# Performance work log

Hardware: AMD Instinct MI355X
Metric: run time of the kernel (lower is better)

The kernel has to match this reference:

```python
import jax, jax.numpy as jnp
import numpy as np

VOCAB, E, H, L, N = 32000, 256, 512, 512, 64


def setup_inputs() -> dict:
    key = jax.random.key(0)
    ks = jax.random.split(key, 8)
    s_in = 1.0 / np.sqrt(H + E)
    return {
        "x": jax.random.randint(ks[0], (L, N), 0, VOCAB),
        "emb": jax.random.normal(ks[1], (VOCAB, E), dtype=jnp.float32),
        # weights stored (in, out); math identical to torch Linear with W.T
        "Wz": jax.random.uniform(ks[2], (H + E, H), jnp.float32, -s_in, s_in),
        "bz": jax.random.uniform(ks[3], (H,), jnp.float32, -s_in, s_in),
        "Wr": jax.random.uniform(ks[4], (H + E, H), jnp.float32, -s_in, s_in),
        "br": jax.random.uniform(ks[5], (H,), jnp.float32, -s_in, s_in),
        "Wh": jax.random.uniform(ks[6], (H + E, H), jnp.float32, -s_in, s_in),
        "bh": jax.random.uniform(ks[7], (H,), jnp.float32, -s_in, s_in),
    }


def reference(x, emb, Wz, bz, Wr, br, Wh, bh):
    # x: (L, N) int indices -> embedded once: (L, N, E)
    xe = emb[x]
    h0 = jnp.zeros((x.shape[1], Wz.shape[1]), dtype=emb.dtype)

    def step(h, e_t):
        hx = jnp.concatenate([h, e_t], axis=1)            # (N, H+E)
        z = jax.nn.sigmoid(hx @ Wz + bz)                  # update gate
        r = jax.nn.sigmoid(hx @ Wr + br)                  # reset gate
        rhx = jnp.concatenate([r * h, e_t], axis=1)
        h_tilde = jnp.tanh(rhx @ Wh + bh)
        h_new = (1.0 - z) * h + z * h_tilde
        return h_new, h_new

    _, hs = jax.lax.scan(step, h0, xe)                    # hs: (L, N, H)
    return hs
```

## Files before the change

kernel.cpp:

```cpp
#include <hip/hip_runtime.h>


#define LSTEPS 512
#define NBATCH 64
#define HDIM   512
#define EDIM   256
#define KDIM   768
#define NBLK   32
#define TPB    256

typedef _Float16 f16x8 __attribute__((ext_vector_type(8)));
typedef float    f32x4 __attribute__((ext_vector_type(4)));

__device__ __forceinline__ float sigm(float x){ return 1.0f/(1.0f+__expf(-x)); }
__device__ __forceinline__ float tanh_fast(float x){
  float e = __expf(2.0f*x);
  return 1.0f - 2.0f/(e + 1.0f);
}

__global__ void prep_w(const float* __restrict__ Wz, const float* __restrict__ Wr,
                       const float* __restrict__ Wh, _Float16* __restrict__ wbuf){
  int tid = blockIdx.x*256 + threadIdx.x;
  int g   = tid / (HDIM*KDIM);
  int rem = tid - g*(HDIM*KDIM);
  int j   = rem / KDIM;
  int k   = rem - j*KDIM;
  const float* W = (g==0) ? Wz : ((g==1) ? Wr : Wh);
  wbuf[tid] = (_Float16)W[(size_t)k*HDIM + j];
}

__global__ void prep_emb(const int* __restrict__ x, const float* __restrict__ emb,
                         _Float16* __restrict__ ebuf){
  int tid = blockIdx.x*256 + threadIdx.x;
  int k4  = tid & 63;
  int tn  = tid >> 6;
  int row = x[tn];
  const float4 v = *(const float4*)(emb + (size_t)row*EDIM + (k4<<2));
  union { _Float16 h[4]; uint2 u; } p;
  p.h[0] = (_Float16)v.x; p.h[1] = (_Float16)v.y;
  p.h[2] = (_Float16)v.z; p.h[3] = (_Float16)v.w;
  *(uint2*)(ebuf + (size_t)tn*EDIM + (k4<<2)) = p.u;
}

__device__ __forceinline__ void gbar(unsigned* cnt, unsigned target){
  __syncthreads();
  if (threadIdx.x == 0){
    __hip_atomic_fetch_add(cnt, 1u, __ATOMIC_RELEASE, __HIP_MEMORY_SCOPE_AGENT);
    while (__hip_atomic_load(cnt, __ATOMIC_RELAXED, __HIP_MEMORY_SCOPE_AGENT) < target){}
    __builtin_amdgcn_fence(__ATOMIC_ACQUIRE, "agent");
  }
  __syncthreads();
}

__global__ __launch_bounds__(TPB) void gru_persist(
    const _Float16* __restrict__ wbuf,
    const _Float16* __restrict__ ebuf,
    const float* __restrict__ bz, const float* __restrict__ br, const float* __restrict__ bh,
    _Float16* __restrict__ hbuf,
    _Float16* __restrict__ rhbuf,
    float* __restrict__ hf,
    float* __restrict__ out,
    unsigned* __restrict__ cnt)
{
  __shared__ char wlds[3*16*1536];
  const int jbase = blockIdx.x * 16;

  for (int cidx = threadIdx.x; cidx < 3*16*96; cidx += TPB){
    int g   = cidx / (16*96);
    int rem = cidx - g*(16*96);
    int col = rem / 96;
    int kch = rem - col*96;
    const uint4 v = *(const uint4*)(wbuf + ((size_t)(g*HDIM + jbase + col))*KDIM + kch*8);
    int off = (((g*16 + col)*1536) + kch*16) ^ ((col & 7) << 4);
    *(uint4*)(wlds + off) = v;
  }
  __syncthreads();

  const int lane = threadIdx.x & 63;
  const int wave = threadIdx.x >> 6;
  const int c15  = lane & 15;
  const int kgrp = lane >> 4;
  const int jcol = jbase + c15;
  const int mt   = wave;
  const int arow = mt*16 + c15;
  const int n0   = mt*16 + kgrp*4;
  const int swz  = (c15 & 7) << 4;
  const int linz = (( 0*16 + c15)*1536) + kgrp*16;
  const int linr = ((1*16 + c15)*1536) + kgrp*16;
  const int linh = ((2*16 + c15)*1536) + kgrp*16;
  const float bzj = bz[jcol];
  const float brj = br[jcol];
  const float bhj = bh[jcol];

  unsigned gen = 0;
  for (int t = 0; t < LSTEPS; ++t){
    const _Float16* et = ebuf + (size_t)t*(NBATCH*EDIM);

    f32x4 accz = {0.f,0.f,0.f,0.f};
    f32x4 accr = {0.f,0.f,0.f,0.f};
    {
      const _Float16* ah = hbuf + arow*HDIM + kgrp*8;
      const _Float16* ae = et   + arow*EDIM + kgrp*8;
      #pragma unroll
      for (int kc = 0; kc < 16; ++kc){
        f16x8 a  = *(const f16x8*)(ah + kc*32);
        f16x8 bzv = *(const f16x8*)(wlds + ((linz + kc*64) ^ swz));
        f16x8 brv = *(const f16x8*)(wlds + ((linr + kc*64) ^ swz));
        accz = __builtin_amdgcn_mfma_f32_16x16x32_f16(a, bzv, accz, 0, 0, 0);
        accr = __builtin_amdgcn_mfma_f32_16x16x32_f16(a, brv, accr, 0, 0, 0);
      }
      #pragma unroll
      for (int kc = 0; kc < 8; ++kc){
        f16x8 a  = *(const f16x8*)(ae + kc*32);
        f16x8 bzv = *(const f16x8*)(wlds + ((linz + (16+kc)*64) ^ swz));
        f16x8 brv = *(const f16x8*)(wlds + ((linr + (16+kc)*64) ^ swz));
        accz = __builtin_amdgcn_mfma_f32_16x16x32_f16(a, bzv, accz, 0, 0, 0);
        accr = __builtin_amdgcn_mfma_f32_16x16x32_f16(a, brv, accr, 0, 0, 0);
      }
    }
    float zreg[4];
    #pragma unroll
    for (int i = 0; i < 4; ++i){
      zreg[i]  = sigm(accz[i] + bzj);
      float r  = sigm(accr[i] + brj);
      float hp = hf[(n0+i)*HDIM + jcol];
      rhbuf[(n0+i)*HDIM + jcol] = (_Float16)(r * hp);
    }
    ++gen; gbar(cnt, NBLK*gen);

    f32x4 acch = {0.f,0.f,0.f,0.f};
    {
      const _Float16* ar = rhbuf + arow*HDIM + kgrp*8;
      const _Float16* ae = et    + arow*EDIM + kgrp*8;
      #pragma unroll
      for (int kc = 0; kc < 16; ++kc){
        f16x8 a  = *(const f16x8*)(ar + kc*32);
        f16x8 bh_ = *(const f16x8*)(wlds + ((linh + kc*64) ^ swz));
        acch = __builtin_amdgcn_mfma_f32_16x16x32_f16(a, bh_, acch, 0, 0, 0);
      }
      #pragma unroll
      for (int kc = 0; kc < 8; ++kc){
        f16x8 a  = *(const f16x8*)(ae + kc*32);
        f16x8 bh_ = *(const f16x8*)(wlds + ((linh + (16+kc)*64) ^ swz));
        acch = __builtin_amdgcn_mfma_f32_16x16x32_f16(a, bh_, acch, 0, 0, 0);
      }
    }
    #pragma unroll
    for (int i = 0; i < 4; ++i){
      float ht = tanh_fast(acch[i] + bhj);
      int   n  = n0 + i;
      float hp = hf[n*HDIM + jcol];
      float hn = hp + zreg[i]*(ht - hp);
      out[((size_t)t*NBATCH + n)*HDIM + jcol] = hn;
      hf[n*HDIM + jcol]   = hn;
      hbuf[n*HDIM + jcol] = (_Float16)hn;
    }
    ++gen; gbar(cnt, NBLK*gen);
  }
}

extern "C" void kernel_launch(void* const* d_in, const int* in_sizes, int n_in,
                              void* d_out, int out_size, void* d_ws, size_t ws_size,
                              hipStream_t stream) {
  const int*   x   = (const int*)  d_in[0];
  const float* emb = (const float*)d_in[1];
  const float* Wz  = (const float*)d_in[2];
  const float* bz  = (const float*)d_in[3];
  const float* Wr  = (const float*)d_in[4];
  const float* br  = (const float*)d_in[5];
  const float* Wh  = (const float*)d_in[6];
  const float* bh  = (const float*)d_in[7];
  float* out = (float*)d_out;
  char*  ws  = (char*)d_ws;

  size_t off = 0;
  unsigned*  cnt   = (unsigned*)(ws + off); off += 256;
  float*     hf    = (float*)   (ws + off); off += (size_t)NBATCH*HDIM*4;
  _Float16*  hbuf  = (_Float16*)(ws + off); off += (size_t)NBATCH*HDIM*2;
  size_t zero_bytes = off;
  _Float16*  rhbuf = (_Float16*)(ws + off); off += (size_t)NBATCH*HDIM*2;
  _Float16*  wbuf  = (_Float16*)(ws + off); off += (size_t)3*HDIM*KDIM*2;
  _Float16*  ebuf  = (_Float16*)(ws + off); off += (size_t)LSTEPS*NBATCH*EDIM*2;

  hipMemsetAsync(ws, 0, zero_bytes, stream);

  prep_w  <<<(3*HDIM*KDIM)/256,          256, 0, stream>>>(Wz, Wr, Wh, wbuf);
  prep_emb<<<(LSTEPS*NBATCH*EDIM/4)/256, 256, 0, stream>>>(x, emb, ebuf);
  gru_persist<<<NBLK, TPB, 0, stream>>>(wbuf, ebuf, bz, br, bh,
                                        hbuf, rhbuf, hf, out, cnt);
}
```

Before: 6.396 ms.

## Replace counter grid barrier with per-block flags and overlap embedding MFMAs

Swaps the single atomic-counter grid barrier for per-block generation flags that a wave polls in parallel with an all-lane check. The embedding part of each gate matmul is moved ahead of the wait so it overlaps barrier latency. The fp32 hidden-state buffer in global memory is replaced by per-thread registers, and hidden/reset outputs are packed into 32-bit stores via a lane shuffle. This cuts global round-trips and serialisation on the critical recurrent path, at the cost of subtler memory-ordering reasoning: flag-based sync with relaxed stores could expose races, for example a block overwriting hbuf while a slower block is still reading it.

```diff
diff --git a/kernel.cpp b/kernel.cpp
--- a/kernel.cpp
+++ b/kernel.cpp
@@ -16,6 +16,9 @@
 __device__ __forceinline__ float tanh_fast(float x){
   float e = __expf(2.0f*x);
   return 1.0f - 2.0f/(e + 1.0f);
+}
+__device__ __forceinline__ unsigned f16b(float x){
+  union { _Float16 h; unsigned short u; } c; c.h = (_Float16)x; return (unsigned)c.u;
 }
 
 __global__ void prep_w(const float* __restrict__ Wz, const float* __restrict__ Wr,
@@ -42,14 +45,36 @@
   *(uint2*)(ebuf + (size_t)tn*EDIM + (k4<<2)) = p.u;
 }
 
-__device__ __forceinline__ void gbar(unsigned* cnt, unsigned target){
-  __syncthreads();
-  if (threadIdx.x == 0){
-    __hip_atomic_fetch_add(cnt, 1u, __ATOMIC_RELEASE, __HIP_MEMORY_SCOPE_AGENT);
-    while (__hip_atomic_load(cnt, __ATOMIC_RELAXED, __HIP_MEMORY_SCOPE_AGENT) < target){}
-    __builtin_amdgcn_fence(__ATOMIC_ACQUIRE, "agent");
-  }
-  __syncthreads();
+__device__ __forceinline__ void wait_flags(unsigned* flags, unsigned target){
+  const int l = threadIdx.x & 63;
+  for (;;){
+    unsigned v = target;
+    if (l < NBLK) v = __hip_atomic_load(&flags[l], __ATOMIC_RELAXED, __HIP_MEMORY_SCOPE_AGENT);
+    if (__all(v >= target)) break;
+  }
+  __builtin_amdgcn_fence(__ATOMIC_ACQUIRE, "agent");
+}
+
+__device__ __forceinline__ void store_x(_Float16* buf, int jc2, int n0, int lane,
+                                        float v0, float v1, float v2, float v3){
+  unsigned p01 = f16b(v0) | (f16b(v1) << 16);
+  unsigned p23 = f16b(v2) | (f16b(v3) << 16);
+  unsigned q01 = __shfl_xor(p01, 1, 64);
+  unsigned q23 = __shfl_xor(p23, 1, 64);
+  unsigned w0, w1; int r0;
+  if (lane & 1){
+    w0 = (q23 & 0xffffu) | (p23 << 16);
+    w1 = (q23 >> 16)     | (p23 & 0xffff0000u);
+    r0 = n0 + 2;
+  } else {
+    w0 = (p01 & 0xffffu) | (q01 << 16);
+    w1 = (p01 >> 16)     | (q01 & 0xffff0000u);
+    r0 = n0;
+  }
+  __hip_atomic_store((unsigned*)(buf + (size_t)r0*HDIM + jc2),     w0,
+                     __ATOMIC_RELAXED, __HIP_MEMORY_SCOPE_AGENT);
+  __hip_atomic_store((unsigned*)(buf + (size_t)(r0+1)*HDIM + jc2), w1,
+                     __ATOMIC_RELAXED, __HIP_MEMORY_SCOPE_AGENT);
 }
 
 __global__ __launch_bounds__(TPB) void gru_persist(
@@ -58,9 +83,8 @@
     const float* __restrict__ bz, const float* __restrict__ br, const float* __restrict__ bh,
     _Float16* __restrict__ hbuf,
     _Float16* __restrict__ rhbuf,
-    float* __restrict__ hf,
     float* __restrict__ out,
-    unsigned* __restrict__ cnt)
+    unsigned* __restrict__ flags)
 {
   __shared__ char wlds[3*16*1536];
   const int jbase = blockIdx.x * 16;
@@ -81,81 +105,87 @@
   const int c15  = lane & 15;
   const int kgrp = lane >> 4;
   const int jcol = jbase + c15;
-  const int mt   = wave;
-  const int arow = mt*16 + c15;
-  const int n0   = mt*16 + kgrp*4;
+  const int jc2  = jcol & ~1;
+  const int arow = wave*16 + c15;
+  const int n0   = wave*16 + kgrp*4;
   const int swz  = (c15 & 7) << 4;
-  const int linz = (( 0*16 + c15)*1536) + kgrp*16;
-  const int linr = ((1*16 + c15)*1536) + kgrp*16;
-  const int linh = ((2*16 + c15)*1536) + kgrp*16;
+  const int linz = ((      c15)*1536) + kgrp*16;
+  const int linr = ((16  + c15)*1536) + kgrp*16;
+  const int linh = ((32  + c15)*1536) + kgrp*16;
   const float bzj = bz[jcol];
   const float brj = br[jcol];
   const float bhj = bh[jcol];
+  float hreg[4] = {0.f, 0.f, 0.f, 0.f};
 
   unsigned gen = 0;
   for (int t = 0; t < LSTEPS; ++t){
     const _Float16* et = ebuf + (size_t)t*(NBATCH*EDIM);
+    const _Float16* ae = et + arow*EDIM + kgrp*8;
 
     f32x4 accz = {0.f,0.f,0.f,0.f};
     f32x4 accr = {0.f,0.f,0.f,0.f};
+    #pragma unroll
+    for (int kc = 0; kc < 8; ++kc){
+      f16x8 a   = *(const f16x8*)(ae + kc*32);
+      f16x8 bzv = *(const f16x8*)(wlds + ((linz + (16+kc)*64) ^ swz));
+      f16x8 brv = *(const f16x8*)(wlds + ((linr + (16+kc)*64) ^ swz));
+      accz = __builtin_amdgcn_mfma_f32_16x16x32_f16(a, bzv, accz, 0, 0, 0);
+      accr = __builtin_amdgcn_mfma_f32_16x16x32_f16(a, brv, accr, 0, 0, 0);
+    }
+    wait_flags(flags, gen);
     {
       const _Float16* ah = hbuf + arow*HDIM + kgrp*8;
-      const _Float16* ae = et   + arow*EDIM + kgrp*8;
       #pragma unroll
       for (int kc = 0; kc < 16; ++kc){
-        f16x8 a  = *(const f16x8*)(ah + kc*32);
+        f16x8 a   = *(const f16x8*)(ah + kc*32);
         f16x8 bzv = *(const f16x8*)(wlds + ((linz + kc*64) ^ swz));
         f16x8 brv = *(const f16x8*)(wlds + ((linr + kc*64) ^ swz));
         accz = __builtin_amdgcn_mfma_f32_16x16x32_f16(a, bzv, accz, 0, 0, 0);
         accr = __builtin_amdgcn_mfma_f32_16x16x32_f16(a, brv, accr, 0, 0, 0);
       }
-      #pragma unroll
-      for (int kc = 0; kc < 8; ++kc){
-        f16x8 a  = *(const f16x8*)(ae + kc*32);
-        f16x8 bzv = *(const f16x8*)(wlds + ((linz + (16+kc)*64) ^ swz));
-        f16x8 brv = *(const f16x8*)(wlds + ((linr + (16+kc)*64) ^ swz));
-        accz = __builtin_amdgcn_mfma_f32_16x16x32_f16(a, bzv, accz, 0, 0, 0);
-        accr = __builtin_amdgcn_mfma_f32_16x16x32_f16(a, brv, accr, 0, 0, 0);
-      }
-    }
-    float zreg[4];
+    }
+    float zreg[4], rh[4];
     #pragma unroll
     for (int i = 0; i < 4; ++i){
-      zreg[i]  = sigm(accz[i] + bzj);
-      float r  = sigm(accr[i] + brj);
-      float hp = hf[(n0+i)*HDIM + jcol];
-      rhbuf[(n0+i)*HDIM + jcol] = (_Float16)(r * hp);
-    }
-    ++gen; gbar(cnt, NBLK*gen);
+      zreg[i] = sigm(accz[i] + bzj);
+      rh[i]   = sigm(accr[i] + brj) * hreg[i];
+    }
+    store_x(rhbuf, jc2, n0, lane, rh[0], rh[1], rh[2], rh[3]);
+    __syncthreads();
+    if (threadIdx.x == 0)
+      __hip_atomic_store(&flags[blockIdx.x], gen+1,
+                         __ATOMIC_RELEASE, __HIP_MEMORY_SCOPE_AGENT);
 
     f32x4 acch = {0.f,0.f,0.f,0.f};
+    #pragma unroll
+    for (int kc = 0; kc < 8; ++kc){
+      f16x8 a   = *(const f16x8*)(ae + kc*32);
+      f16x8 bhv = *(const f16x8*)(wlds + ((linh + (16+kc)*64) ^ swz));
+      acch = __builtin_amdgcn_mfma_f32_16x16x32_f16(a, bhv, acch, 0, 0, 0);
+    }
+    wait_flags(flags, gen+1);
     {
       const _Float16* ar = rhbuf + arow*HDIM + kgrp*8;
-      const _Float16* ae = et    + arow*EDIM + kgrp*8;
       #pragma unroll
       for (int kc = 0; kc < 16; ++kc){
-        f16x8 a  = *(const f16x8*)(ar + kc*32);
-        f16x8 bh_ = *(const f16x8*)(wlds + ((linh + kc*64) ^ swz));
-        acch = __builtin_amdgcn_mfma_f32_16x16x32_f16(a, bh_, acch, 0, 0, 0);
-      }
-      #pragma unroll
-      for (int kc = 0; kc < 8; ++kc){
-        f16x8 a  = *(const f16x8*)(ae + kc*32);
-        f16x8 bh_ = *(const f16x8*)(wlds + ((linh + (16+kc)*64) ^ swz));
-        acch = __builtin_amdgcn_mfma_f32_16x16x32_f16(a, bh_, acch, 0, 0, 0);
+        f16x8 a   = *(const f16x8*)(ar + kc*32);
+        f16x8 bhv = *(const f16x8*)(wlds + ((linh + kc*64) ^ swz));
+        acch = __builtin_amdgcn_mfma_f32_16x16x32_f16(a, bhv, acch, 0, 0, 0);
       }
     }
     #pragma unroll
     for (int i = 0; i < 4; ++i){
       float ht = tanh_fast(acch[i] + bhj);
-      int   n  = n0 + i;
-      float hp = hf[n*HDIM + jcol];
-      float hn = hp + zreg[i]*(ht - hp);
-      out[((size_t)t*NBATCH + n)*HDIM + jcol] = hn;
-      hf[n*HDIM + jcol]   = hn;
-      hbuf[n*HDIM + jcol] = (_Float16)hn;
-    }
-    ++gen; gbar(cnt, NBLK*gen);
+      float hn = hreg[i] + zreg[i]*(ht - hreg[i]);
+      hreg[i] = hn;
+      out[((size_t)t*NBATCH + (n0+i))*HDIM + jcol] = hn;
+    }
+    store_x(hbuf, jc2, n0, lane, hreg[0], hreg[1], hreg[2], hreg[3]);
+    __syncthreads();
+    if (threadIdx.x == 0)
+      __hip_atomic_store(&flags[blockIdx.x], gen+2,
+                         __ATOMIC_RELEASE, __HIP_MEMORY_SCOPE_AGENT);
+    gen += 2;
   }
 }
 
@@ -174,8 +204,7 @@
   char*  ws  = (char*)d_ws;
 
   size_t off = 0;
-  unsigned*  cnt   = (unsigned*)(ws + off); off += 256;
-  float*     hf    = (float*)   (ws + off); off += (size_t)NBATCH*HDIM*4;
+  unsigned*  flags = (unsigned*)(ws + off); off += 256;
   _Float16*  hbuf  = (_Float16*)(ws + off); off += (size_t)NBATCH*HDIM*2;
   size_t zero_bytes = off;
   _Float16*  rhbuf = (_Float16*)(ws + off); off += (size_t)NBATCH*HDIM*2;
@@ -187,5 +216,5 @@
   prep_w  <<<(3*HDIM*KDIM)/256,          256, 0, stream>>>(Wz, Wr, Wh, wbuf);
   prep_emb<<<(LSTEPS*NBATCH*EDIM/4)/256, 256, 0, stream>>>(x, emb, ebuf);
   gru_persist<<<NBLK, TPB, 0, stream>>>(wbuf, ebuf, bz, br, bh,
-                                        hbuf, rhbuf, hf, out, cnt);
-}
+                                        hbuf, rhbuf, out, flags);
+}
```

Result: faster. 5.934 ms (-7.2%).

## Replace persistent kernel grid barriers with per-step kernel launches

Applied to the files above, without the earlier changes.

Drops the persistent kernel that relied on atomic-counter grid barriers and LDS-resident weights. Each time step now launches two small kernels, one for the z/r gates and one for the candidate and state update, which read weights straight from global memory (L2). Kernel boundaries replace the spin barriers, at the cost of 1024 launches and reloading the weights every step.

```diff
diff --git a/kernel.cpp b/kernel.cpp
--- a/kernel.cpp
+++ b/kernel.cpp
@@ -42,120 +42,104 @@
   *(uint2*)(ebuf + (size_t)tn*EDIM + (k4<<2)) = p.u;
 }
 
-__device__ __forceinline__ void gbar(unsigned* cnt, unsigned target){
-  __syncthreads();
-  if (threadIdx.x == 0){
-    __hip_atomic_fetch_add(cnt, 1u, __ATOMIC_RELEASE, __HIP_MEMORY_SCOPE_AGENT);
-    while (__hip_atomic_load(cnt, __ATOMIC_RELAXED, __HIP_MEMORY_SCOPE_AGENT) < target){}
-    __builtin_amdgcn_fence(__ATOMIC_ACQUIRE, "agent");
-  }
-  __syncthreads();
-}
 
-__global__ __launch_bounds__(TPB) void gru_persist(
+__global__ __launch_bounds__(TPB) void gru_p1(
     const _Float16* __restrict__ wbuf,
     const _Float16* __restrict__ ebuf,
-    const float* __restrict__ bz, const float* __restrict__ br, const float* __restrict__ bh,
-    _Float16* __restrict__ hbuf,
-    _Float16* __restrict__ rhbuf,
-    float* __restrict__ hf,
-    float* __restrict__ out,
-    unsigned* __restrict__ cnt)
+    const _Float16* __restrict__ hx,
+    const float* __restrict__ hf,
+    const float* __restrict__ bz, const float* __restrict__ br,
+    float* __restrict__ zbuf,
+    _Float16* __restrict__ rhx,
+    int t)
 {
-  __shared__ char wlds[3*16*1536];
-  const int jbase = blockIdx.x * 16;
-
-  for (int cidx = threadIdx.x; cidx < 3*16*96; cidx += TPB){
-    int g   = cidx / (16*96);
-    int rem = cidx - g*(16*96);
-    int col = rem / 96;
-    int kch = rem - col*96;
-    const uint4 v = *(const uint4*)(wbuf + ((size_t)(g*HDIM + jbase + col))*KDIM + kch*8);
-    int off = (((g*16 + col)*1536) + kch*16) ^ ((col & 7) << 4);
-    *(uint4*)(wlds + off) = v;
-  }
-  __syncthreads();
-
   const int lane = threadIdx.x & 63;
   const int wave = threadIdx.x >> 6;
   const int c15  = lane & 15;
   const int kgrp = lane >> 4;
-  const int jcol = jbase + c15;
-  const int mt   = wave;
-  const int arow = mt*16 + c15;
-  const int n0   = mt*16 + kgrp*4;
-  const int swz  = (c15 & 7) << 4;
-  const int linz = (( 0*16 + c15)*1536) + kgrp*16;
-  const int linr = ((1*16 + c15)*1536) + kgrp*16;
-  const int linh = ((2*16 + c15)*1536) + kgrp*16;
+  const int jcol = blockIdx.x*16 + c15;
+  const int arow = wave*16 + c15;
+  const int n0   = wave*16 + kgrp*4;
+  const _Float16* ah = hx + (size_t)arow*HDIM + kgrp*8;
+  const _Float16* ae = ebuf + ((size_t)t*NBATCH + arow)*EDIM + kgrp*8;
+  const _Float16* wz = wbuf + (size_t)(0*HDIM + jcol)*KDIM + kgrp*8;
+  const _Float16* wr = wbuf + (size_t)(1*HDIM + jcol)*KDIM + kgrp*8;
+
+  f32x4 accz = {0.f,0.f,0.f,0.f};
+  f32x4 accr = {0.f,0.f,0.f,0.f};
+  #pragma unroll
+  for (int kc = 0; kc < 16; ++kc){
+    f16x8 a   = *(const f16x8*)(ah + kc*32);
+    f16x8 bzv = *(const f16x8*)(wz + kc*32);
+    f16x8 brv = *(const f16x8*)(wr + kc*32);
+    accz = __builtin_amdgcn_mfma_f32_16x16x32_f16(a, bzv, accz, 0, 0, 0);
+    accr = __builtin_amdgcn_mfma_f32_16x16x32_f16(a, brv, accr, 0, 0, 0);
+  }
+  #pragma unroll
+  for (int kc = 0; kc < 8; ++kc){
+    f16x8 a   = *(const f16x8*)(ae + kc*32);
+    f16x8 bzv = *(const f16x8*)(wz + (16+kc)*32);
+    f16x8 brv = *(const f16x8*)(wr + (16+kc)*32);
+    accz = __builtin_amdgcn_mfma_f32_16x16x32_f16(a, bzv, accz, 0, 0, 0);
+    accr = __builtin_amdgcn_mfma_f32_16x16x32_f16(a, brv, accr, 0, 0, 0);
+  }
   const float bzj = bz[jcol];
   const float brj = br[jcol];
+  #pragma unroll
+  for (int i = 0; i < 4; ++i){
+    int n = n0 + i;
+    float hp = hf[(size_t)n*HDIM + jcol];
+    zbuf[(size_t)n*HDIM + jcol] = sigm(accz[i] + bzj);
+    rhx [(size_t)n*HDIM + jcol] = (_Float16)(sigm(accr[i] + brj) * hp);
+  }
+}
+
+__global__ __launch_bounds__(TPB) void gru_p2(
+    const _Float16* __restrict__ wbuf,
+    const _Float16* __restrict__ ebuf,
+    const _Float16* __restrict__ rhx,
+    const float* __restrict__ zbuf,
+    const float* __restrict__ bh,
+    float* __restrict__ hf,
+    _Float16* __restrict__ hx,
+    float* __restrict__ out,
+    int t)
+{
+  const int lane = threadIdx.x & 63;
+  const int wave = threadIdx.x >> 6;
+  const int c15  = lane & 15;
+  const int kgrp = lane >> 4;
+  const int jcol = blockIdx.x*16 + c15;
+  const int arow = wave*16 + c15;
+  const int n0   = wave*16 + kgrp*4;
+  const _Float16* ar = rhx + (size_t)arow*HDIM + kgrp*8;
+  const _Float16* ae = ebuf + ((size_t)t*NBATCH + arow)*EDIM + kgrp*8;
+  const _Float16* wh = wbuf + (size_t)(2*HDIM + jcol)*KDIM + kgrp*8;
+
+  f32x4 acch = {0.f,0.f,0.f,0.f};
+  #pragma unroll
+  for (int kc = 0; kc < 16; ++kc){
+    f16x8 a   = *(const f16x8*)(ar + kc*32);
+    f16x8 bhv = *(const f16x8*)(wh + kc*32);
+    acch = __builtin_amdgcn_mfma_f32_16x16x32_f16(a, bhv, acch, 0, 0, 0);
+  }
+  #pragma unroll
+  for (int kc = 0; kc < 8; ++kc){
+    f16x8 a   = *(const f16x8*)(ae + kc*32);
+    f16x8 bhv = *(const f16x8*)(wh + (16+kc)*32);
+    acch = __builtin_amdgcn_mfma_f32_16x16x32_f16(a, bhv, acch, 0, 0, 0);
+  }
   const float bhj = bh[jcol];
-
-  unsigned gen = 0;
-  for (int t = 0; t < LSTEPS; ++t){
-    const _Float16* et = ebuf + (size_t)t*(NBATCH*EDIM);
-
-    f32x4 accz = {0.f,0.f,0.f,0.f};
-    f32x4 accr = {0.f,0.f,0.f,0.f};
-    {
-      const _Float16* ah = hbuf + arow*HDIM + kgrp*8;
-      const _Float16* ae = et   + arow*EDIM + kgrp*8;
-      #pragma unroll
-      for (int kc = 0; kc < 16; ++kc){
-        f16x8 a  = *(const f16x8*)(ah + kc*32);
-        f16x8 bzv = *(const f16x8*)(wlds + ((linz + kc*64) ^ swz));
-        f16x8 brv = *(const f16x8*)(wlds + ((linr + kc*64) ^ swz));
-        accz = __builtin_amdgcn_mfma_f32_16x16x32_f16(a, bzv, accz, 0, 0, 0);
-        accr = __builtin_amdgcn_mfma_f32_16x16x32_f16(a, brv, accr, 0, 0, 0);
-      }
-      #pragma unroll
-      for (int kc = 0; kc < 8; ++kc){
-        f16x8 a  = *(const f16x8*)(ae + kc*32);
-        f16x8 bzv = *(const f16x8*)(wlds + ((linz + (16+kc)*64) ^ swz));
-        f16x8 brv = *(const f16x8*)(wlds + ((linr + (16+kc)*64) ^ swz));
-        accz = __builtin_amdgcn_mfma_f32_16x16x32_f16(a, bzv, accz, 0, 0, 0);
-        accr = __builtin_amdgcn_mfma_f32_16x16x32_f16(a, brv, accr, 0, 0, 0);
-      }
-    }
-    float zreg[4];
-    #pragma unroll
-    for (int i = 0; i < 4; ++i){
-      zreg[i]  = sigm(accz[i] + bzj);
-      float r  = sigm(accr[i] + brj);
-      float hp = hf[(n0+i)*HDIM + jcol];
-      rhbuf[(n0+i)*HDIM + jcol] = (_Float16)(r * hp);
-    }
-    ++gen; gbar(cnt, NBLK*gen);
-
-    f32x4 acch = {0.f,0.f,0.f,0.f};
-    {
-      const _Float16* ar = rhbuf + arow*HDIM + kgrp*8;
-      const _Float16* ae = et    + arow*EDIM + kgrp*8;
-      #pragma unroll
-      for (int kc = 0; kc < 16; ++kc){
-        f16x8 a  = *(const f16x8*)(ar + kc*32);
-        f16x8 bh_ = *(const f16x8*)(wlds + ((linh + kc*64) ^ swz));
-        acch = __builtin_amdgcn_mfma_f32_16x16x32_f16(a, bh_, acch, 0, 0, 0);
-      }
-      #pragma unroll
-      for (int kc = 0; kc < 8; ++kc){
-        f16x8 a  = *(const f16x8*)(ae + kc*32);
-        f16x8 bh_ = *(const f16x8*)(wlds + ((linh + (16+kc)*64) ^ swz));
-        acch = __builtin_amdgcn_mfma_f32_16x16x32_f16(a, bh_, acch, 0, 0, 0);
-      }
-    }
-    #pragma unroll
-    for (int i = 0; i < 4; ++i){
-      float ht = tanh_fast(acch[i] + bhj);
-      int   n  = n0 + i;
-      float hp = hf[n*HDIM + jcol];
-      float hn = hp + zreg[i]*(ht - hp);
-      out[((size_t)t*NBATCH + n)*HDIM + jcol] = hn;
-      hf[n*HDIM + jcol]   = hn;
-      hbuf[n*HDIM + jcol] = (_Float16)hn;
-    }
-    ++gen; gbar(cnt, NBLK*gen);
+  #pragma unroll
+  for (int i = 0; i < 4; ++i){
+    int n = n0 + i;
+    float ht = tanh_fast(acch[i] + bhj);
+    float hp = hf[(size_t)n*HDIM + jcol];
+    float z  = zbuf[(size_t)n*HDIM + jcol];
+    float hn = hp + z*(ht - hp);
+    hf[(size_t)n*HDIM + jcol] = hn;
+    hx[(size_t)n*HDIM + jcol] = (_Float16)hn;
+    out[((size_t)t*NBATCH + n)*HDIM + jcol] = hn;
   }
 }
 
@@ -174,18 +158,21 @@
   char*  ws  = (char*)d_ws;
 
   size_t off = 0;
-  unsigned*  cnt   = (unsigned*)(ws + off); off += 256;
-  float*     hf    = (float*)   (ws + off); off += (size_t)NBATCH*HDIM*4;
-  _Float16*  hbuf  = (_Float16*)(ws + off); off += (size_t)NBATCH*HDIM*2;
+  _Float16* hx   = (_Float16*)(ws + off); off += (size_t)NBATCH*HDIM*2;
+  float*    hf   = (float*)   (ws + off); off += (size_t)NBATCH*HDIM*4;
   size_t zero_bytes = off;
-  _Float16*  rhbuf = (_Float16*)(ws + off); off += (size_t)NBATCH*HDIM*2;
-  _Float16*  wbuf  = (_Float16*)(ws + off); off += (size_t)3*HDIM*KDIM*2;
-  _Float16*  ebuf  = (_Float16*)(ws + off); off += (size_t)LSTEPS*NBATCH*EDIM*2;
+  _Float16* rhx  = (_Float16*)(ws + off); off += (size_t)NBATCH*HDIM*2;
+  float*    zbuf = (float*)   (ws + off); off += (size_t)NBATCH*HDIM*4;
+  _Float16* wbuf = (_Float16*)(ws + off); off += (size_t)3*HDIM*KDIM*2;
+  _Float16* ebuf = (_Float16*)(ws + off); off += (size_t)LSTEPS*NBATCH*EDIM*2;
 
   hipMemsetAsync(ws, 0, zero_bytes, stream);
 
   prep_w  <<<(3*HDIM*KDIM)/256,          256, 0, stream>>>(Wz, Wr, Wh, wbuf);
   prep_emb<<<(LSTEPS*NBATCH*EDIM/4)/256, 256, 0, stream>>>(x, emb, ebuf);
-  gru_persist<<<NBLK, TPB, 0, stream>>>(wbuf, ebuf, bz, br, bh,
-                                        hbuf, rhbuf, hf, out, cnt);
+
+  for (int t = 0; t < LSTEPS; ++t){
+    gru_p1<<<NBLK, TPB, 0, stream>>>(wbuf, ebuf, hx, hf, bz, br, zbuf, rhx, t);
+    gru_p2<<<NBLK, TPB, 0, stream>>>(wbuf, ebuf, rhx, zbuf, bh, hf, hx, out, t);
+  }
 }
```

Result: slower. 8.942 ms (+39.8%).
